# Kernel optimization log

Hardware: AMD Instinct MI355X
Metric: run time of the kernel (lower is better)

Reference implementation:

```python
import jax, jax.numpy as jnp
import numpy as np

EPS = 1e-12  # F.normalize eps
WIN_SIZE = 200
WIN_STEP = 30  # eval mode (training uses 10)
N_WIN = 30     # 31 windows from length-1100 axis, last one dropped


def setup_inputs() -> dict:
    key = jax.random.key(0)
    ks = jax.random.split(key, 6)
    dim, K, out_dim = 128, 64, 256
    N, H, W = 8, 16, 900
    s = 1.0 / np.sqrt(dim)
    return {
        "x": jax.random.normal(ks[0], (N, dim, H, W), dtype=jnp.float32),
        "cluster_centers": jax.random.uniform(ks[1], (K, dim), dtype=jnp.float32),
        "conv_w": jax.random.normal(ks[2], (K, dim), dtype=jnp.float32) * s,
        "conv_b": jax.random.normal(ks[3], (K,), dtype=jnp.float32) * s,
        "mlp_w": jax.random.normal(ks[4], (out_dim, K * dim), dtype=jnp.float32) * s,
        "mlp_b": jax.random.normal(ks[5], (out_dim,), dtype=jnp.float32) * s,
    }


def _l2norm(v, axis):
    return v / jnp.clip(jnp.linalg.norm(v, axis=axis, keepdims=True), EPS)


def reference(x, cluster_centers, conv_w, conv_b, mlp_w, mlp_b):
    N, C, H, W = x.shape
    K = conv_w.shape[0]
    # 1x1 conv -> soft assignment, softmax over clusters (dim=1 after view(N,K,HW))
    logits = jnp.einsum('nchw,kc->nkhw', x, conv_w) + conv_b[None, :, None, None]
    a = jax.nn.softmax(logits, axis=1)  # (N,K,H,W)
    # Fused weighted residual sum over H (torch sums dim=-2 of (N,K,C,H,W)):
    # vlad_pre[n,k,c,w] = sum_h a[n,k,h,w]*x[n,c,h,w] - centers[k,c]*sum_h a[n,k,h,w]
    wx = jnp.einsum('nkhw,nchw->nkcw', a, x)               # (N,K,C,W)
    asum = a.sum(axis=2)                                    # (N,K,W)
    res = wx - cluster_centers[None, :, :, None] * asum[:, :, None, :]
    # circular pad along yaw: [800:] ++ all ++ [:100] -> length 1100
    res = jnp.concatenate([res[..., 800:], res, res[..., :100]], axis=-1)
    # sliding-window sum, size 200 step 30, drop last window -> 30 windows
    cs = jnp.cumsum(res, axis=-1)
    cs = jnp.concatenate([jnp.zeros(res.shape[:-1] + (1,), res.dtype), cs], axis=-1)
    starts = jnp.arange(N_WIN) * WIN_STEP
    win = cs[..., starts + WIN_SIZE] - cs[..., starts]      # (N,K,C,30)
    vlad = jnp.transpose(win, (0, 3, 1, 2)).reshape(N * N_WIN, K, C)
    vlad = _l2norm(vlad, axis=2)                            # intra-norm per cluster
    vlad = _l2norm(vlad.reshape(N * N_WIN, K * C), axis=1)  # global norm
    out = vlad @ mlp_w.T + mlp_b
    out = _l2norm(out, axis=1)
    return out.reshape(N, N_WIN, -1)
```

## Files before the change

### kernel.cpp

```cpp
#include <hip/hip_runtime.h>
#include <cstddef>

#define EPSF 1e-12f
#define NCB 90
#define NT 30
#define ODIM 256
#define DDIM 8192

typedef unsigned short u16;
typedef __attribute__((ext_vector_type(8))) short short8;
typedef __attribute__((ext_vector_type(4))) float float4v;

__device__ inline u16 f2bf(float f) {
  union { float f; unsigned u; } v; v.f = f;
  unsigned r = v.u + 0x7FFFu + ((v.u >> 16) & 1u);
  return (u16)(r >> 16);
}
__device__ inline float bf2f(u16 h) {
  union { unsigned u; float f; } v; v.u = ((unsigned)h) << 16;
  return v.f;
}

__global__ __launch_bounds__(256, 3) void k1_assign(
    const float* __restrict__ x,
    const float* __restrict__ conv_w,
    const float* __restrict__ conv_b,
    float* __restrict__ P,
    float* __restrict__ PA)
{
  __shared__ u16 xtf[4160];
  __shared__ u16 xf[5120];
  __shared__ float As[64 * 33];
  __shared__ u16 afr[2048];
  __shared__ float invs[32];
  __shared__ float pasum[256];

  const int bx0 = blockIdx.x;
  const int id = (bx0 & 7) * 90 + (bx0 >> 3);
  const int n = id / NCB, cb = id - n * NCB;
  const int t = threadIdx.x;
  const int lane = t & 63;
  const int w = t >> 6;

  const float* xn = x + (size_t)n * 1843200 + cb * 10;

  const int colt = w & 1;
  const int kt0 = w >> 1;
  const float bk0 = conv_b[kt0 * 16 + (lane & 15)];
  const float bk1 = conv_b[(kt0 + 2) * 16 + (lane & 15)];

  short8 w0h[4], w0l[4], w1h[4], w1l[4];
  {
    int kr0 = kt0 * 16 + (lane & 15);
    int kr1 = kr0 + 32;
    int cbase = (lane >> 4) << 3;
#pragma unroll
    for (int cb32 = 0; cb32 < 4; ++cb32) {
      const float* wp0 = conv_w + (size_t)kr0 * 128 + cb32 * 32 + cbase;
      const float* wp1 = conv_w + (size_t)kr1 * 128 + cb32 * 32 + cbase;
      union { u16 u[8]; short8 v; } hh, ll;
#pragma unroll
      for (int j = 0; j < 8; ++j) {
        float fv = wp0[j];
        u16 h = f2bf(fv);
        hh.u[j] = h;
        ll.u[j] = f2bf(fv - bf2f(h));
      }
      w0h[cb32] = hh.v; w0l[cb32] = ll.v;
#pragma unroll
      for (int j = 0; j < 8; ++j) {
        float fv = wp1[j];
        u16 h = f2bf(fv);
        hh.u[j] = h;
        ll.u[j] = f2bf(fv - bf2f(h));
      }
      w1h[cb32] = hh.v; w1l[cb32] = ll.v;
    }
  }

  float4v pacc[8];
#pragma unroll
  for (int i = 0; i < 8; ++i) pacc[i] = (float4v){0.f, 0.f, 0.f, 0.f};
  float pak = 0.f;

  float2 xr[8];
#pragma unroll
  for (int s = 0; s < 8; ++s) {
    int e2 = t + 256 * s;
    int c = e2 >> 4, p = e2 & 15;
    int cl = 2 * p;
    int h = cl / 10, wi = cl - 10 * h;
    xr[s] = *(const float2*)(xn + (size_t)c * 14400 + h * 900 + wi);
  }

  for (int cc = 0; cc < 5; ++cc) {
    __syncthreads();
#pragma unroll
    for (int s = 0; s < 8; ++s) {
      int e2 = t + 256 * s;
      int c = e2 >> 4, p = e2 & 15;
      int cl = 2 * p;
      u16 h0 = f2bf(xr[s].x), h1 = f2bf(xr[s].y);
      int ip = (c >> 4) * 640 + (p >> 2) * 160 + (c & 15) * 8 + (cl & 7);
      ushort2 pr; pr.x = h0; pr.y = h1;
      *(ushort2*)&xf[ip] = pr;
      int F = (p >> 3) * 4 + (c >> 5);
      int L = (((c >> 3) & 3) << 4) + (cl & 15);
      int i0 = F * 520 + L * 8 + (c & 7);
      xtf[i0] = h0;
      xtf[i0 + 8] = h1;
    }
    if (cc < 4) {
#pragma unroll
      for (int s = 0; s < 8; ++s) {
        int e2 = t + 256 * s;
        int c = e2 >> 4, p = e2 & 15;
        int g = (cc + 1) * 32 + 2 * p;
        int h = g / 10, wi = g - 10 * h;
        xr[s] = *(const float2*)(xn + (size_t)c * 14400 + h * 900 + wi);
      }
    }
    __syncthreads();

    {
      float4v d0 = (float4v){0.f, 0.f, 0.f, 0.f};
      float4v d1 = (float4v){0.f, 0.f, 0.f, 0.f};
#pragma unroll
      for (int cb32 = 0; cb32 < 4; ++cb32) {
        short8 xa = *(short8*)&xtf[(colt * 4 + cb32) * 520 + lane * 8];
        d0 = __builtin_amdgcn_mfma_f32_16x16x32_bf16(xa, w0h[cb32], d0, 0, 0, 0);
        d0 = __builtin_amdgcn_mfma_f32_16x16x32_bf16(xa, w0l[cb32], d0, 0, 0, 0);
        d1 = __builtin_amdgcn_mfma_f32_16x16x32_bf16(xa, w1h[cb32], d1, 0, 0, 0);
        d1 = __builtin_amdgcn_mfma_f32_16x16x32_bf16(xa, w1l[cb32], d1, 0, 0, 0);
      }
      int colb = colt * 16 + ((lane >> 4) << 2);
      int kr0 = kt0 * 16 + (lane & 15);
      int kr1 = kr0 + 32;
#pragma unroll
      for (int r = 0; r < 4; ++r) {
        As[kr0 * 33 + colb + r] = d0[r] + bk0;
        As[kr1 * 33 + colb + r] = d1[r] + bk1;
      }
    }
    __syncthreads();

    {
      const int col8 = lane & 7;
      const int kq = lane >> 3;
      const int colg = w * 8 + col8;
      float m = -3.4e38f;
#pragma unroll
      for (int i = 0; i < 8; ++i) m = fmaxf(m, As[(kq * 8 + i) * 33 + colg]);
      m = fmaxf(m, __shfl_xor(m, 8));
      m = fmaxf(m, __shfl_xor(m, 16));
      m = fmaxf(m, __shfl_xor(m, 32));
      float s = 0.f;
#pragma unroll
      for (int i = 0; i < 8; ++i) {
        int a = (kq * 8 + i) * 33 + colg;
        float e = __expf(As[a] - m);
        As[a] = e;
        s += e;
      }
      s += __shfl_xor(s, 8);
      s += __shfl_xor(s, 16);
      s += __shfl_xor(s, 32);
      if (kq == 0) invs[w * 8 + col8] = 1.f / s;
    }
    {
      union { u16 u[8]; short8 v; } cvt;
      float paks = 0.f;
#pragma unroll
      for (int j = 0; j < 8; ++j) {
        float a = As[lane * 33 + w * 8 + j] * invs[w * 8 + j];
        paks += a;
        cvt.u[j] = f2bf(a);
      }
      pak += paks;
      int dst = ((lane >> 4) * 64 + (w << 4) + (lane & 15)) * 8;
      *(short8*)&afr[dst] = cvt.v;
    }
    __syncthreads();

    {
      short8 aa = *(short8*)&afr[(w * 64 + lane) * 8];
#pragma unroll
      for (int ct = 0; ct < 8; ++ct) {
        short8 xb = *(short8*)&xf[ct * 640 + (lane >> 4) * 160 + (lane & 15) * 8];
        pacc[ct] = __builtin_amdgcn_mfma_f32_16x16x32_bf16(aa, xb, pacc[ct], 0, 0, 0);
      }
    }
  }

  float* Pp = P + (size_t)(n * NCB + cb) * DDIM;
  {
    int krow = w * 16 + ((lane >> 4) << 2);
    int c0 = lane & 15;
#pragma unroll
    for (int ct = 0; ct < 8; ++ct)
#pragma unroll
      for (int r = 0; r < 4; ++r)
        Pp[(krow + r) * 128 + ct * 16 + c0] = pacc[ct][r];
  }
  pasum[t] = pak;
  __syncthreads();
  if (t < 64)
    PA[(size_t)(n * NCB + cb) * 64 + t] =
        pasum[t] + pasum[64 + t] + pasum[128 + t] + pasum[192 + t];
}

__global__ __launch_bounds__(256) void k2_vlad(
    const float* __restrict__ P, const float* __restrict__ PA,
    const float* __restrict__ centers, u16* __restrict__ vlad16,
    float* __restrict__ gss)
{
  __shared__ float Ak[16];
  __shared__ float red[4];
  const int bx0 = blockIdx.x;
  const int id = (bx0 & 7) * 120 + (bx0 >> 3);
  const int n = id / 120;
  const int rem = id - n * 120;
  const int wt = rem >> 2, eb = rem & 3;
  const int win = n * NT + wt;
  const int t = threadIdx.x;

  if (t < 64) {
    int kk = t >> 2, ii = t & 3;
    float s = 0.f;
#pragma unroll
    for (int ss = 0; ss < 5; ++ss) {
      int i = ii + 4 * ss;
      int cb = (3 * wt + 80 + i) % 90;
      s += PA[((size_t)n * NCB + cb) * 64 + eb * 16 + kk];
    }
    s += __shfl_xor(s, 1);
    s += __shfl_xor(s, 2);
    if (ii == 0) Ak[kk] = s;
  }
  __syncthreads();

  const int e0 = eb * 2048 + t * 8;
  float v[8];
#pragma unroll
  for (int j = 0; j < 8; ++j) v[j] = 0.f;
#pragma unroll 5
  for (int i = 0; i < 20; ++i) {
    int cb = (3 * wt + 80 + i) % 90;
    const float* Pp = P + ((size_t)n * NCB + cb) * DDIM + e0;
    float4 u0 = *(const float4*)Pp;
    float4 u1 = *(const float4*)(Pp + 4);
    v[0] += u0.x; v[1] += u0.y; v[2] += u0.z; v[3] += u0.w;
    v[4] += u1.x; v[5] += u1.y; v[6] += u1.z; v[7] += u1.w;
  }
  const float A = Ak[t >> 4];
  const float* ce = centers + e0;
  float ss8 = 0.f;
#pragma unroll
  for (int j = 0; j < 8; ++j) {
    float val = v[j] - ce[j] * A;
    v[j] = val;
    ss8 += val * val;
  }
  float ssg = ss8;
  ssg += __shfl_xor(ssg, 1);
  ssg += __shfl_xor(ssg, 2);
  ssg += __shfl_xor(ssg, 4);
  ssg += __shfl_xor(ssg, 8);
  float rn = 1.f / fmaxf(sqrtf(ssg), EPSF);
  float ts = ss8 * rn * rn;
  ts += __shfl_xor(ts, 1);
  ts += __shfl_xor(ts, 2);
  ts += __shfl_xor(ts, 4);
  ts += __shfl_xor(ts, 8);
  ts += __shfl_xor(ts, 16);
  ts += __shfl_xor(ts, 32);
  if ((t & 63) == 0) red[t >> 6] = ts;
  __syncthreads();
  if (t == 0) gss[(size_t)win * 4 + eb] = red[0] + red[1] + red[2] + red[3];

  union { u16 u[8]; short8 s; } o;
#pragma unroll
  for (int j = 0; j < 8; ++j) o.u[j] = f2bf(v[j] * rn);
  *(short8*)(vlad16 + (size_t)win * DDIM + e0) = o.s;
}

__global__ __launch_bounds__(256) void k3_gemm(
    const u16* __restrict__ vlad16, const float* __restrict__ gss,
    const float* __restrict__ mlp_w, float* __restrict__ part)
{
  __shared__ float ga[16];
  const int bx = blockIdx.x;
  const int rt = bx % 15;
  const int h = bx / 15;
  const int ot = h & 1;
  const int ks = h >> 1;
  const int t = threadIdx.x;
  const int lane = t & 63;
  const int w = t >> 6;

  if (t < 16) {
    int r = rt * 16 + t;
    float s = gss[r * 4] + gss[r * 4 + 1] + gss[r * 4 + 2] + gss[r * 4 + 3];
    ga[t] = 1.f / fmaxf(sqrtf(s), EPSF);
  }
  __syncthreads();

  const int m = lane & 15;
  const int kg = lane >> 4;
  const int d0 = ks * 256 + kg * 8;
  const u16* arow = vlad16 + (size_t)(rt * 16 + m) * DDIM + d0;

  float4v acc[2];
#pragma unroll
  for (int i = 0; i < 2; ++i) acc[i] = (float4v){0.f, 0.f, 0.f, 0.f};

#pragma unroll
  for (int ko = 0; ko < 8; ++ko) {
    short8 a = *(const short8*)(arow + ko * 32);
#pragma unroll
    for (int nt = 0; nt < 2; ++nt) {
      int o = ot * 128 + w * 32 + nt * 16 + m;
      const float* wrow = mlp_w + (size_t)o * DDIM + d0 + ko * 32;
      float4 u0 = *(const float4*)wrow;
      float4 u1 = *(const float4*)(wrow + 4);
      union { u16 u[8]; short8 v; } bb;
      bb.u[0] = f2bf(u0.x); bb.u[1] = f2bf(u0.y); bb.u[2] = f2bf(u0.z); bb.u[3] = f2bf(u0.w);
      bb.u[4] = f2bf(u1.x); bb.u[5] = f2bf(u1.y); bb.u[6] = f2bf(u1.z); bb.u[7] = f2bf(u1.w);
      acc[nt] = __builtin_amdgcn_mfma_f32_16x16x32_bf16(a, bb.v, acc[nt], 0, 0, 0);
    }
  }

  float g4[4];
#pragma unroll
  for (int r = 0; r < 4; ++r) g4[r] = ga[kg * 4 + r];
  float* pp = part + ((size_t)ks * 240 + rt * 16) * ODIM;
#pragma unroll
  for (int nt = 0; nt < 2; ++nt) {
    int o = ot * 128 + w * 32 + nt * 16 + m;
#pragma unroll
    for (int r = 0; r < 4; ++r)
      pp[(kg * 4 + r) * ODIM + o] = acc[nt][r] * g4[r];
  }
}

__global__ __launch_bounds__(256) void k4_out(
    const float* __restrict__ part, const float* __restrict__ bias,
    float* __restrict__ out)
{
  __shared__ float red[4];
  const int r = blockIdx.x;
  const int o = threadIdx.x;
  float v = bias[o];
#pragma unroll
  for (int s = 0; s < 32; ++s) v += part[((size_t)s * 240 + r) * ODIM + o];
  float ss = v * v;
  ss += __shfl_xor(ss, 32);
  ss += __shfl_xor(ss, 16);
  ss += __shfl_xor(ss, 8);
  ss += __shfl_xor(ss, 4);
  ss += __shfl_xor(ss, 2);
  ss += __shfl_xor(ss, 1);
  if ((o & 63) == 0) red[o >> 6] = ss;
  __syncthreads();
  float total = red[0] + red[1] + red[2] + red[3];
  out[(size_t)r * ODIM + o] = v / fmaxf(sqrtf(total), EPSF);
}

extern "C" void kernel_launch(void* const* d_in, const int* in_sizes, int n_in,
                              void* d_out, int out_size, void* d_ws, size_t ws_size,
                              hipStream_t stream) {
  const float* x       = (const float*)d_in[0];
  const float* centers = (const float*)d_in[1];
  const float* conv_w  = (const float*)d_in[2];
  const float* conv_b  = (const float*)d_in[3];
  const float* mlp_w   = (const float*)d_in[4];
  const float* mlp_b   = (const float*)d_in[5];
  float* out = (float*)d_out;

  float* ws     = (float*)d_ws;
  float* P      = ws;
  float* PA     = ws + 5898240;
  u16*   vlad16 = (u16*)(ws + 5944320);
  float* gss    = (float*)(ws + 6927360);
  float* part   = ws;

  k1_assign<<<dim3(8 * NCB),    dim3(256), 0, stream>>>(x, conv_w, conv_b, P, PA);
  k2_vlad  <<<dim3(8 * NT * 4), dim3(256), 0, stream>>>(P, PA, centers, vlad16, gss);
  k3_gemm  <<<dim3(960),        dim3(256), 0, stream>>>(vlad16, gss, mlp_w, part);
  k4_out   <<<dim3(240),        dim3(256), 0, stream>>>(part, mlp_b, out);
}
```

Baseline: 172.4 us.

## Split k1 channel output across two blocks, pre-cast MLP weights to bf16

k1_assign now launches twice as many blocks, each computing the weighted sum for half of the 128 channels. Both halves still compute the full softmax assignment redundantly, but each holds half the accumulators and LDS, allowing 4 blocks per CU. A new k0_wcast kernel converts mlp_w to bf16 once into workspace, so k3_gemm reads half the bytes and skips per-element conversion; k3's block indexing is also remapped per XCD. The cost is an extra launch, a full weight pass, and duplicated logit and softmax work in k1.

```diff
diff --git a/kernel.cpp b/kernel.cpp
--- a/kernel.cpp
+++ b/kernel.cpp
@@ -21,7 +21,7 @@
   return v.f;
 }
 
-__global__ __launch_bounds__(256, 3) void k1_assign(
+__global__ __launch_bounds__(256, 4) void k1_assign(
     const float* __restrict__ x,
     const float* __restrict__ conv_w,
     const float* __restrict__ conv_b,
@@ -29,15 +29,17 @@
     float* __restrict__ PA)
 {
   __shared__ u16 xtf[4160];
-  __shared__ u16 xf[5120];
+  __shared__ u16 xf[2560];
   __shared__ float As[64 * 33];
   __shared__ u16 afr[2048];
   __shared__ float invs[32];
   __shared__ float pasum[256];
 
   const int bx0 = blockIdx.x;
-  const int id = (bx0 & 7) * 90 + (bx0 >> 3);
-  const int n = id / NCB, cb = id - n * NCB;
+  const int n = bx0 & 7;
+  const int r2 = bx0 >> 3;
+  const int cb = r2 >> 1;
+  const int chb = r2 & 1;
   const int t = threadIdx.x;
   const int lane = t & 63;
   const int w = t >> 6;
@@ -78,9 +80,9 @@
     }
   }
 
-  float4v pacc[8];
-#pragma unroll
-  for (int i = 0; i < 8; ++i) pacc[i] = (float4v){0.f, 0.f, 0.f, 0.f};
+  float4v pacc[4];
+#pragma unroll
+  for (int i = 0; i < 4; ++i) pacc[i] = (float4v){0.f, 0.f, 0.f, 0.f};
   float pak = 0.f;
 
   float2 xr[8];
@@ -101,9 +103,11 @@
       int c = e2 >> 4, p = e2 & 15;
       int cl = 2 * p;
       u16 h0 = f2bf(xr[s].x), h1 = f2bf(xr[s].y);
-      int ip = (c >> 4) * 640 + (p >> 2) * 160 + (c & 15) * 8 + (cl & 7);
-      ushort2 pr; pr.x = h0; pr.y = h1;
-      *(ushort2*)&xf[ip] = pr;
+      if ((s >> 2) == chb) {
+        int ip = ((c >> 4) & 3) * 640 + (p >> 2) * 160 + (c & 15) * 8 + (cl & 7);
+        ushort2 pr; pr.x = h0; pr.y = h1;
+        *(ushort2*)&xf[ip] = pr;
+      }
       int F = (p >> 3) * 4 + (c >> 5);
       int L = (((c >> 3) & 3) << 4) + (cl & 15);
       int i0 = F * 520 + L * 8 + (c & 7);
@@ -185,7 +189,7 @@
     {
       short8 aa = *(short8*)&afr[(w * 64 + lane) * 8];
 #pragma unroll
-      for (int ct = 0; ct < 8; ++ct) {
+      for (int ct = 0; ct < 4; ++ct) {
         short8 xb = *(short8*)&xf[ct * 640 + (lane >> 4) * 160 + (lane & 15) * 8];
         pacc[ct] = __builtin_amdgcn_mfma_f32_16x16x32_bf16(aa, xb, pacc[ct], 0, 0, 0);
       }
@@ -197,16 +201,18 @@
     int krow = w * 16 + ((lane >> 4) << 2);
     int c0 = lane & 15;
 #pragma unroll
-    for (int ct = 0; ct < 8; ++ct)
+    for (int ct = 0; ct < 4; ++ct)
 #pragma unroll
       for (int r = 0; r < 4; ++r)
-        Pp[(krow + r) * 128 + ct * 16 + c0] = pacc[ct][r];
-  }
-  pasum[t] = pak;
-  __syncthreads();
-  if (t < 64)
-    PA[(size_t)(n * NCB + cb) * 64 + t] =
-        pasum[t] + pasum[64 + t] + pasum[128 + t] + pasum[192 + t];
+        Pp[(krow + r) * 128 + chb * 64 + ct * 16 + c0] = pacc[ct][r];
+  }
+  if (chb == 0) {
+    pasum[t] = pak;
+    __syncthreads();
+    if (t < 64)
+      PA[(size_t)(n * NCB + cb) * 64 + t] =
+          pasum[t] + pasum[64 + t] + pasum[128 + t] + pasum[192 + t];
+  }
 }
 
 __global__ __launch_bounds__(256) void k2_vlad(
@@ -284,14 +290,28 @@
   *(short8*)(vlad16 + (size_t)win * DDIM + e0) = o.s;
 }
 
+__global__ __launch_bounds__(256) void k0_wcast(
+    const float* __restrict__ mlp_w, u16* __restrict__ wbf)
+{
+  const size_t i = (size_t)(blockIdx.x * 256 + threadIdx.x) * 8;
+  float4 u0 = *(const float4*)(mlp_w + i);
+  float4 u1 = *(const float4*)(mlp_w + i + 4);
+  union { u16 u[8]; short8 s; } o;
+  o.u[0] = f2bf(u0.x); o.u[1] = f2bf(u0.y); o.u[2] = f2bf(u0.z); o.u[3] = f2bf(u0.w);
+  o.u[4] = f2bf(u1.x); o.u[5] = f2bf(u1.y); o.u[6] = f2bf(u1.z); o.u[7] = f2bf(u1.w);
+  *(short8*)(wbf + i) = o.s;
+}
+
 __global__ __launch_bounds__(256) void k3_gemm(
     const u16* __restrict__ vlad16, const float* __restrict__ gss,
-    const float* __restrict__ mlp_w, float* __restrict__ part)
+    const u16* __restrict__ wbf, float* __restrict__ part)
 {
   __shared__ float ga[16];
   const int bx = blockIdx.x;
-  const int rt = bx % 15;
-  const int h = bx / 15;
+  const int xcd = bx & 7;
+  const int i6 = bx >> 3;
+  const int h = xcd * 8 + (i6 & 7);
+  const int rt = i6 >> 3;
   const int ot = h & 1;
   const int ks = h >> 1;
   const int t = threadIdx.x;
@@ -320,13 +340,8 @@
 #pragma unroll
     for (int nt = 0; nt < 2; ++nt) {
       int o = ot * 128 + w * 32 + nt * 16 + m;
-      const float* wrow = mlp_w + (size_t)o * DDIM + d0 + ko * 32;
-      float4 u0 = *(const float4*)wrow;
-      float4 u1 = *(const float4*)(wrow + 4);
-      union { u16 u[8]; short8 v; } bb;
-      bb.u[0] = f2bf(u0.x); bb.u[1] = f2bf(u0.y); bb.u[2] = f2bf(u0.z); bb.u[3] = f2bf(u0.w);
-      bb.u[4] = f2bf(u1.x); bb.u[5] = f2bf(u1.y); bb.u[6] = f2bf(u1.z); bb.u[7] = f2bf(u1.w);
-      acc[nt] = __builtin_amdgcn_mfma_f32_16x16x32_bf16(a, bb.v, acc[nt], 0, 0, 0);
+      short8 bv = *(const short8*)(wbf + (size_t)o * DDIM + d0 + ko * 32);
+      acc[nt] = __builtin_amdgcn_mfma_f32_16x16x32_bf16(a, bv, acc[nt], 0, 0, 0);
     }
   }
 
@@ -383,9 +398,11 @@
   u16*   vlad16 = (u16*)(ws + 5944320);
   float* gss    = (float*)(ws + 6927360);
   float* part   = ws;
-
-  k1_assign<<<dim3(8 * NCB),    dim3(256), 0, stream>>>(x, conv_w, conv_b, P, PA);
-  k2_vlad  <<<dim3(8 * NT * 4), dim3(256), 0, stream>>>(P, PA, centers, vlad16, gss);
-  k3_gemm  <<<dim3(960),        dim3(256), 0, stream>>>(vlad16, gss, mlp_w, part);
-  k4_out   <<<dim3(240),        dim3(256), 0, stream>>>(part, mlp_b, out);
-}
+  u16*   wbf    = (u16*)(ws + 1966080);
+
+  k1_assign<<<dim3(8 * NCB * 2), dim3(256), 0, stream>>>(x, conv_w, conv_b, P, PA);
+  k2_vlad  <<<dim3(8 * NT * 4),  dim3(256), 0, stream>>>(P, PA, centers, vlad16, gss);
+  k0_wcast <<<dim3(1024),        dim3(256), 0, stream>>>(mlp_w, wbf);
+  k3_gemm  <<<dim3(960),         dim3(256), 0, stream>>>(vlad16, gss, wbf, part);
+  k4_out   <<<dim3(240),         dim3(256), 0, stream>>>(part, mlp_b, out);
+}
```

Result: slower. 247.3 us (+43.4%).
